# Optimization experiments

Measured on AMD Instinct MI355X. Metric: run time of the kernel, lower is better.

The kernel has to match this reference:

```python
import jax, jax.numpy as jnp
import numpy as np

B, M, E, H = 256, 196, 1024, 8
Dh = E // H          # 128 = att_mid_dim[0]
MID = 64             # att_mid_dim[1]
ALPHA = 1.3          # CELU alpha
EPS = 1e-5


def group_norm(x, w, b, groups=H, eps=EPS):
    # x: [N, C]; torch GroupNorm over channel groups
    N, C = x.shape
    xg = x.reshape(N, groups, C // groups)
    mu = xg.mean(-1, keepdims=True)
    var = xg.var(-1, keepdims=True)
    xn = ((xg - mu) * jax.lax.rsqrt(var + eps)).reshape(N, C)
    return xn * w + b


def proj(x, W, b, gw, gb):
    # Linear -> CELU(1.3) -> GroupNorm(H)
    return group_norm(jax.nn.celu(x @ W + b, alpha=ALPHA), gw, gb)


def setup_inputs() -> dict:
    key0 = jax.random.key(0)
    ks = jax.random.split(key0, 16)
    d = {}
    d["query"] = jax.random.normal(ks[0], (B, E), jnp.float32)
    d["key"] = jax.random.normal(ks[1], (B, M, E), jnp.float32)
    d["mask"] = jax.random.randint(ks[2], (B, M), 0, 2, jnp.int32)
    d["value1"] = jax.random.normal(ks[3], (B, E), jnp.float32)
    d["value2"] = jax.random.normal(ks[4], (B, M, E), jnp.float32)
    s = 0.02
    for i, nm in enumerate(["q", "k", "v1", "v2"]):
        d[f"W{nm}"] = jax.random.normal(ks[5 + i], (E, E), jnp.float32) * s
        d[f"b{nm}"] = jnp.zeros((E,), jnp.float32)
        d[f"g{nm}_w"] = jnp.ones((E,), jnp.float32)
        d[f"g{nm}_b"] = jnp.zeros((E,), jnp.float32)
    d["Wb"] = jax.random.normal(ks[9], (Dh, MID), jnp.float32) * s
    d["bb"] = jnp.zeros((MID,), jnp.float32)
    d["Ws"] = jax.random.normal(ks[10], (MID, 1), jnp.float32) * s
    d["bs"] = jnp.zeros((1,), jnp.float32)
    d["Wc"] = jax.random.normal(ks[11], (MID, Dh), jnp.float32) * s
    d["bc"] = jnp.zeros((Dh,), jnp.float32)
    return d


def reference(query, key, mask, value1, value2,
              Wq, bq, gq_w, gq_b, Wk, bk, gk_w, gk_b,
              Wv1, bv1, gv1_w, gv1_b, Wv2, bv2, gv2_w, gv2_b,
              Wb, bb, Ws, bs, Wc, bc):
    # input projections (dropout layers are identity at eval)
    q = proj(query, Wq, bq, gq_w, gq_b).reshape(B, H, Dh)
    v1 = proj(value1, Wv1, bv1, gv1_w, gv1_b).reshape(B, H, Dh)
    k = proj(key.reshape(-1, E), Wk, bk, gk_w, gk_b).reshape(B, M, H, Dh).transpose(0, 2, 1, 3)   # [B,H,M,Dh]
    v2 = proj(value2.reshape(-1, E), Wv2, bv2, gv2_w, gv2_b).reshape(B, M, H, Dh).transpose(0, 2, 1, 3)

    # SCAttDec
    att_map = q[:, :, None, :] * k                                # [B,H,M,Dh]
    hidden = jax.nn.relu(att_map @ Wb + bb)                       # [B,H,M,MID]
    maskf = mask.astype(hidden.dtype)                             # [B,M]
    mext = maskf[:, None, :, None]                                # [B,1,M,1]
    att_map_pool = jnp.sum(hidden * mext, axis=2) / jnp.sum(mext, axis=2)   # [B,H,MID]

    alpha_spatial = (hidden @ Ws + bs)[..., 0]                    # [B,H,M]
    alpha_spatial = jnp.where(mask[:, None, :] == 0, -1e9, alpha_spatial)
    alpha_spatial = jax.nn.softmax(alpha_spatial, axis=-1)
    v2_pooled = jnp.einsum("bhm,bhmd->bhd", alpha_spatial, v2)    # [B,H,Dh]

    alpha_channel = jax.nn.sigmoid(att_map_pool @ Wc + bc)        # [B,H,Dh]
    attn = v1 * v2_pooled * alpha_channel                         # [B,H,Dh]
    return attn.reshape(B, H * Dh)
```

## Files before the change

### kernel.cpp

```cpp
#include <hip/hip_runtime.h>

typedef unsigned short u16;
typedef unsigned int u32;
typedef __attribute__((ext_vector_type(8))) short short8;
typedef __attribute__((ext_vector_type(4))) float floatx4;

#define E_ 1024
#define B_ 256
#define M_ 196
#define H_ 8
#define DH_ 128
#define MID_ 64

__device__ __forceinline__ u16 f2bf(float f){
  union { float f; u32 u; } v; v.f = f;
  return (u16)((v.u + (((v.u >> 16) & 1u) + 0x7fffu)) >> 16);
}
__device__ __forceinline__ float bf2f(u16 h){
  union { u32 u; float f; } v; v.u = ((u32)h) << 16;
  return v.f;
}
__device__ __forceinline__ u32 pack_bf2(float a, float b){
  u32 ua = __float_as_uint(a) + 0x8000u;
  u32 ub = __float_as_uint(b) + 0x8000u;
  return __builtin_amdgcn_perm(ub, ua, 0x07060302);
}
__device__ __forceinline__ void gl_lds16(const void* g, void* l){
  __builtin_amdgcn_global_load_lds(
      (const __attribute__((address_space(1))) u32*)g,
      (__attribute__((address_space(3))) u32*)l, 16, 0, 0);
}

__global__ __launch_bounds__(256) void wconv_kernel(
    const float* __restrict__ Wq, const float* __restrict__ Wk,
    const float* __restrict__ Wv1, const float* __restrict__ Wv2,
    u16* __restrict__ Wt)
{
  __shared__ u16 tile[64][72];
  const float* W = (blockIdx.z == 0) ? Wq : (blockIdx.z == 1) ? Wk
                 : (blockIdx.z == 2) ? Wv1 : Wv2;
  u16* out = Wt + (size_t)blockIdx.z * (E_ * E_);
  int k0 = blockIdx.x * 64, c0 = blockIdx.y * 64;
  int tx = threadIdx.x & 63, ty = threadIdx.x >> 6;
  #pragma unroll
  for (int i = 0; i < 16; i++){
    int k = ty * 16 + i;
    tile[k][tx] = f2bf(W[(size_t)(k0 + k) * E_ + c0 + tx]);
  }
  __syncthreads();
  #pragma unroll
  for (int i = 0; i < 16; i++){
    int c = ty * 16 + i;
    out[(size_t)(c0 + c) * E_ + k0 + tx] = tile[tx][c];
  }
}

__global__ __launch_bounds__(256, 2) void proj_kernel(
    const float* __restrict__ query, const float* __restrict__ key,
    const float* __restrict__ value1, const float* __restrict__ value2,
    const float* __restrict__ bq, const float* __restrict__ gqw, const float* __restrict__ gqb,
    const float* __restrict__ bk, const float* __restrict__ gkw, const float* __restrict__ gkb,
    const float* __restrict__ bv1, const float* __restrict__ gv1w, const float* __restrict__ gv1b,
    const float* __restrict__ bv2, const float* __restrict__ gv2w, const float* __restrict__ gv2b,
    const u16* __restrict__ Wt,
    u16* __restrict__ qout, u16* __restrict__ kout,
    u16* __restrict__ v1out, u16* __restrict__ v2out)
{
  __shared__ float a_lds[128 * 32];
  __shared__ u16  b_lds[256 * 32];

  const int tid = threadIdx.x;
  const int w = tid >> 6, lane = tid & 63, qd = lane >> 4, lr = lane & 15;
  const int rh = w >> 1, ch = w & 1;

  const int mtb = blockIdx.y;
  const float* X; const float *bias, *gw, *gb; u16* out; int row0, matsel;
  if (mtb < 392)      { X = key;    bias = bk;  gw = gkw;  gb = gkb;  out = kout;  row0 = mtb * 128;         matsel = 1; }
  else if (mtb < 784) { X = value2; bias = bv2; gw = gv2w; gb = gv2b; out = v2out; row0 = (mtb - 392) * 128; matsel = 3; }
  else if (mtb < 786) { X = query;  bias = bq;  gw = gqw;  gb = gqb;  out = qout;  row0 = (mtb - 784) * 128; matsel = 0; }
  else                { X = value1; bias = bv1; gw = gv1w; gb = gv1b; out = v1out; row0 = (mtb - 786) * 128; matsel = 2; }
  const int col0 = blockIdx.x * 256;

  const int arow_l = w * 32 + (lane >> 3);
  const int aswz   = ((lane & 7) ^ (lane >> 3)) * 4;
  const float* aSrc = X + (size_t)(row0 + arow_l) * E_ + aswz;
  const int bcol_l = w * 64 + (lane >> 2);
  const u16* bSrc = Wt + (size_t)matsel * (E_ * E_) + (size_t)(col0 + bcol_l) * E_ + (lane & 3) * 8;

  floatx4 acc[4][8];
  #pragma unroll
  for (int i = 0; i < 4; i++)
    #pragma unroll
    for (int j = 0; j < 8; j++){
      floatx4 z = {0.f, 0.f, 0.f, 0.f};
      acc[i][j] = z;
    }

  for (int kt = 0; kt < 32; kt++){
    const int k0 = kt * 32;
    __syncthreads();
    #pragma unroll
    for (int c = 0; c < 4; c++)
      gl_lds16(aSrc + (size_t)c * 8 * E_ + k0, &a_lds[(w * 32 + c * 8) * 32]);
    #pragma unroll
    for (int c = 0; c < 4; c++)
      gl_lds16(bSrc + (size_t)c * 16 * E_ + k0, &b_lds[(w * 64 + c * 16) * 32]);
    __syncthreads();

    short8 bfr[8];
    #pragma unroll
    for (int nt = 0; nt < 8; nt++)
      bfr[nt] = *(const short8*)&b_lds[(ch * 128 + nt * 16 + lr) * 32 + qd * 8];

    const int sw = lr & 7;
    #pragma unroll
    for (int m2 = 0; m2 < 4; m2++){
      const int row = rh * 64 + m2 * 16 + lr;
      float4 f0 = *(const float4*)&a_lds[row * 32 + (((qd << 1)    ) ^ sw) * 4];
      float4 f1 = *(const float4*)&a_lds[row * 32 + (((qd << 1) | 1) ^ sw) * 4];
      union { u32 u[4]; short8 s; } af;
      af.u[0] = pack_bf2(f0.x, f0.y);
      af.u[1] = pack_bf2(f0.z, f0.w);
      af.u[2] = pack_bf2(f1.x, f1.y);
      af.u[3] = pack_bf2(f1.z, f1.w);
      #pragma unroll
      for (int nt = 0; nt < 8; nt++)
        acc[m2][nt] = __builtin_amdgcn_mfma_f32_16x16x32_bf16(af.s, bfr[nt], acc[m2][nt], 0, 0, 0);
    }
  }

  float biasv[8], gwv[8], gbv[8];
  #pragma unroll
  for (int nt = 0; nt < 8; nt++){
    int c = col0 + ch * 128 + nt * 16 + lr;
    biasv[nt] = bias[c]; gwv[nt] = gw[c]; gbv[nt] = gb[c];
  }
  #pragma unroll
  for (int m2 = 0; m2 < 4; m2++){
    #pragma unroll
    for (int r = 0; r < 4; r++){
      float s = 0.f, s2 = 0.f;
      #pragma unroll
      for (int nt = 0; nt < 8; nt++){
        float x = acc[m2][nt][r] + biasv[nt];
        x = (x > 0.f) ? x : 1.3f * expm1f(x * (1.0f / 1.3f));
        acc[m2][nt][r] = x;
        s += x; s2 += x * x;
      }
      #pragma unroll
      for (int off = 1; off < 16; off <<= 1){
        s  += __shfl_xor(s,  off, 64);
        s2 += __shfl_xor(s2, off, 64);
      }
      float mean = s * 0.0078125f;
      float var  = s2 * 0.0078125f - mean * mean;
      float rstd = rsqrtf(var + 1e-5f);
      size_t base = (size_t)(row0 + rh * 64 + m2 * 16 + qd * 4 + r) * E_ + col0 + ch * 128;
      #pragma unroll
      for (int nt = 0; nt < 8; nt++)
        out[base + nt * 16 + lr] = f2bf((acc[m2][nt][r] - mean) * rstd * gwv[nt] + gbv[nt]);
    }
  }
}

__global__ __launch_bounds__(256) void attn_kernel(
    const u16* __restrict__ qproj, const u16* __restrict__ kproj,
    const u16* __restrict__ v1proj, const u16* __restrict__ v2proj,
    const int* __restrict__ mask,
    const float* __restrict__ Wb, const float* __restrict__ bb,
    const float* __restrict__ Ws, const float* __restrict__ bs,
    const float* __restrict__ Wc, const float* __restrict__ bc,
    float* __restrict__ outp)
{
  __shared__ u16 wbt[64 * 136];
  __shared__ float qv[128];
  __shared__ float mrow[208];
  __shared__ float logitv[208];
  __shared__ float hsum_l[4][64];
  __shared__ float wexpv[208];
  __shared__ float poolv[64];
  __shared__ float v2acc[4][128];
  __shared__ float red[8];

  const int tid = threadIdx.x;
  const int w = tid >> 6, lane = tid & 63, qd = lane >> 4, lr = lane & 15;
  const int b = blockIdx.y, h = blockIdx.x;

  const u16* kbase  = kproj  + (size_t)b * M_ * E_ + h * DH_;
  const u16* v2base = v2proj + (size_t)b * M_ * E_ + h * DH_;

  if (tid < 128) qv[tid] = bf2f(qproj[(size_t)b * E_ + h * DH_ + tid]);
  if (tid < 208) mrow[tid] = (tid < M_) ? (float)mask[b * M_ + tid] : 0.f;
  __syncthreads();

  {
    int n = tid & 63, kb = (tid >> 6) * 32;
    #pragma unroll
    for (int kk = 0; kk < 32; kk++)
      wbt[n * 136 + kb + kk] = f2bf(qv[kb + kk] * Wb[(kb + kk) * MID_ + n]);
  }
  __syncthreads();

  float wsv[4], bbv[4];
  #pragma unroll
  for (int nt = 0; nt < 4; nt++){ wsv[nt] = Ws[nt * 16 + lr]; bbv[nt] = bb[nt * 16 + lr]; }
  const float bsv = bs[0];
  float hs[4] = {0, 0, 0, 0};

  for (int mt = w; mt < 13; mt += 4){
    int mrow_g = mt * 16 + lr;
    int mcl = (mrow_g < M_) ? mrow_g : (M_ - 1);
    const u16* arow = kbase + (size_t)mcl * E_;
    floatx4 hacc[4];
    #pragma unroll
    for (int nt = 0; nt < 4; nt++){ floatx4 z = {0.f, 0.f, 0.f, 0.f}; hacc[nt] = z; }
    #pragma unroll
    for (int kc = 0; kc < 4; kc++){
      short8 afr = *(const short8*)(arow + kc * 32 + qd * 8);
      #pragma unroll
      for (int nt = 0; nt < 4; nt++){
        short8 bfr = *(const short8*)&wbt[(nt * 16 + lr) * 136 + kc * 32 + qd * 8];
        hacc[nt] = __builtin_amdgcn_mfma_f32_16x16x32_bf16(afr, bfr, hacc[nt], 0, 0, 0);
      }
    }
    float lp[4] = {0, 0, 0, 0};
    #pragma unroll
    for (int nt = 0; nt < 4; nt++){
      #pragma unroll
      for (int r = 0; r < 4; r++){
        float hv = hacc[nt][r] + bbv[nt];
        hv = fmaxf(hv, 0.f);
        lp[r] += hv * wsv[nt];
        hs[nt] += mrow[mt * 16 + qd * 4 + r] * hv;
      }
    }
    #pragma unroll
    for (int r = 0; r < 4; r++){
      float a = lp[r];
      #pragma unroll
      for (int off = 1; off < 16; off <<= 1) a += __shfl_xor(a, off, 64);
      if (lr == 0) logitv[mt * 16 + qd * 4 + r] = a + bsv;
    }
  }
  #pragma unroll
  for (int nt = 0; nt < 4; nt++){
    hs[nt] += __shfl_xor(hs[nt], 16, 64);
    hs[nt] += __shfl_xor(hs[nt], 32, 64);
  }
  if (lane < 16){
    #pragma unroll
    for (int nt = 0; nt < 4; nt++) hsum_l[w][nt * 16 + lane] = hs[nt];
  }
  __syncthreads();

  if (w == 0){
    float s = 0.f;
    for (int m = lane; m < M_; m += 64) s += mrow[m];
    #pragma unroll
    for (int off = 1; off < 64; off <<= 1) s += __shfl_xor(s, off, 64);
    if (lane == 0) red[0] = s;
  } else if (w == 1){
    float mx = -1e30f;
    for (int m = lane; m < M_; m += 64) if (mrow[m] > 0.5f) mx = fmaxf(mx, logitv[m]);
    #pragma unroll
    for (int off = 1; off < 64; off <<= 1) mx = fmaxf(mx, __shfl_xor(mx, off, 64));
    if (lane == 0) red[1] = mx;
  } else if (w == 2){
    poolv[lane & 63] = hsum_l[0][lane & 63] + hsum_l[1][lane & 63]
                     + hsum_l[2][lane & 63] + hsum_l[3][lane & 63];
  }
  __syncthreads();
  const float cnt = red[0], mx = red[1];
  if (tid < 208)
    wexpv[tid] = (tid < M_ && mrow[tid] > 0.5f) ? expf(logitv[tid] - mx) : 0.f;
  __syncthreads();
  if (w == 0){
    float s = 0.f;
    for (int m = lane; m < M_; m += 64) s += wexpv[m];
    #pragma unroll
    for (int off = 1; off < 64; off <<= 1) s += __shfl_xor(s, off, 64);
    if (lane == 0) red[2] = s;
  } else if (w == 1){
    poolv[lane & 63] = poolv[lane & 63] / cnt;
  }
  __syncthreads();
  const float S = red[2];

  {
    float ac[8] = {0, 0, 0, 0, 0, 0, 0, 0};
    #pragma unroll
    for (int it = 0; it < 13; it++){
      int m = it * 16 + w * 4 + qd;
      if (m < M_){
        float we = wexpv[m];
        uint4 u = *(const uint4*)(v2base + (size_t)m * E_ + lr * 8);
        ac[0] += we * bf2f((u16)(u.x & 0xffff));
        ac[1] += we * bf2f((u16)(u.x >> 16));
        ac[2] += we * bf2f((u16)(u.y & 0xffff));
        ac[3] += we * bf2f((u16)(u.y >> 16));
        ac[4] += we * bf2f((u16)(u.z & 0xffff));
        ac[5] += we * bf2f((u16)(u.z >> 16));
        ac[6] += we * bf2f((u16)(u.w & 0xffff));
        ac[7] += we * bf2f((u16)(u.w >> 16));
      }
    }
    #pragma unroll
    for (int j = 0; j < 8; j++){
      ac[j] += __shfl_xor(ac[j], 16, 64);
      ac[j] += __shfl_xor(ac[j], 32, 64);
    }
    if (qd == 0){
      #pragma unroll
      for (int j = 0; j < 8; j++) v2acc[w][lr * 8 + j] = ac[j];
    }
  }
  __syncthreads();

  if (tid < 128){
    float a = 0.f;
    #pragma unroll 8
    for (int j = 0; j < 64; j++) a += poolv[j] * Wc[j * DH_ + tid];
    float acv = 1.f / (1.f + expf(-(a + bc[tid])));
    float vp = (v2acc[0][tid] + v2acc[1][tid] + v2acc[2][tid] + v2acc[3][tid]) / S;
    float o = bf2f(v1proj[(size_t)b * E_ + h * DH_ + tid]) * vp * acv;
    outp[(size_t)b * E_ + h * DH_ + tid] = o;
  }
}

extern "C" void kernel_launch(void* const* d_in, const int* in_sizes, int n_in,
                              void* d_out, int out_size, void* d_ws, size_t ws_size,
                              hipStream_t stream)
{
  const float* query  = (const float*)d_in[0];
  const float* key    = (const float*)d_in[1];
  const int*   mask   = (const int*)d_in[2];
  const float* value1 = (const float*)d_in[3];
  const float* value2 = (const float*)d_in[4];
  const float* Wq  = (const float*)d_in[5];
  const float* bq  = (const float*)d_in[6];
  const float* gqw = (const float*)d_in[7];
  const float* gqb = (const float*)d_in[8];
  const float* Wk  = (const float*)d_in[9];
  const float* bk  = (const float*)d_in[10];
  const float* gkw = (const float*)d_in[11];
  const float* gkb = (const float*)d_in[12];
  const float* Wv1 = (const float*)d_in[13];
  const float* bv1 = (const float*)d_in[14];
  const float* gv1w= (const float*)d_in[15];
  const float* gv1b= (const float*)d_in[16];
  const float* Wv2 = (const float*)d_in[17];
  const float* bv2 = (const float*)d_in[18];
  const float* gv2w= (const float*)d_in[19];
  const float* gv2b= (const float*)d_in[20];
  const float* Wb  = (const float*)d_in[21];
  const float* bb  = (const float*)d_in[22];
  const float* Ws  = (const float*)d_in[23];
  const float* bs  = (const float*)d_in[24];
  const float* Wc  = (const float*)d_in[25];
  const float* bc  = (const float*)d_in[26];

  const size_t NK = (size_t)B_ * M_;
  u16* kout  = (u16*)d_ws;
  u16* v2out = kout  + NK * E_;
  u16* qout  = v2out + NK * E_;
  u16* v1out = qout  + (size_t)B_ * E_;
  u16* Wt    = v1out + (size_t)B_ * E_;

  dim3 g0(16, 16, 4);
  wconv_kernel<<<g0, 256, 0, stream>>>(Wq, Wk, Wv1, Wv2, Wt);

  dim3 g1(4, 788);
  proj_kernel<<<g1, 256, 0, stream>>>(query, key, value1, value2,
      bq, gqw, gqb, bk, gkw, gkb, bv1, gv1w, gv1b, bv2, gv2w, gv2b,
      Wt, qout, kout, v1out, v2out);

  dim3 g2(H_, B_);
  attn_kernel<<<g2, 256, 0, stream>>>(qout, kout, v1out, v2out, mask,
      Wb, bb, Ws, bs, Wc, bc, (float*)d_out);
}
```

Before: 886.2 us.

## Retile projection GEMM to 128x128 with register-staged bf16 A tiles

The projection GEMM tile shrinks from 128x256 to 128x128 output and the K step grows from 32 to 64. The fp32 A operand is now prefetched into registers, converted to bf16 once per tile, and stored to LDS with an XOR swizzle. Previously each wave reconverted fp32 from LDS on every use. Because each 128-column group now spans two waves, GroupNorm statistics are combined through shared memory, and occupancy is raised to 3 blocks per CU. The cost is twice as many blocks, so the A matrix is read from global memory twice as often, plus an extra barrier in the epilogue.

```diff
diff --git a/kernel.cpp b/kernel.cpp
--- a/kernel.cpp
+++ b/kernel.cpp
@@ -55,7 +55,7 @@
   }
 }
 
-__global__ __launch_bounds__(256, 2) void proj_kernel(
+__global__ __launch_bounds__(256, 3) void proj_kernel(
     const float* __restrict__ query, const float* __restrict__ key,
     const float* __restrict__ value1, const float* __restrict__ value2,
     const float* __restrict__ bq, const float* __restrict__ gqw, const float* __restrict__ gqb,
@@ -66,8 +66,9 @@
     u16* __restrict__ qout, u16* __restrict__ kout,
     u16* __restrict__ v1out, u16* __restrict__ v2out)
 {
-  __shared__ float a_lds[128 * 32];
-  __shared__ u16  b_lds[256 * 32];
+  __shared__ u16 a_lds[128 * 64];
+  __shared__ u16 b_lds[128 * 64];
+  __shared__ float ps[128][2][2];
 
   const int tid = threadIdx.x;
   const int w = tid >> 6, lane = tid & 63, qd = lane >> 4, lr = lane & 15;
@@ -79,60 +80,69 @@
   else if (mtb < 784) { X = value2; bias = bv2; gw = gv2w; gb = gv2b; out = v2out; row0 = (mtb - 392) * 128; matsel = 3; }
   else if (mtb < 786) { X = query;  bias = bq;  gw = gqw;  gb = gqb;  out = qout;  row0 = (mtb - 784) * 128; matsel = 0; }
   else                { X = value1; bias = bv1; gw = gv1w; gb = gv1b; out = v1out; row0 = (mtb - 786) * 128; matsel = 2; }
-  const int col0 = blockIdx.x * 256;
-
-  const int arow_l = w * 32 + (lane >> 3);
-  const int aswz   = ((lane & 7) ^ (lane >> 3)) * 4;
-  const float* aSrc = X + (size_t)(row0 + arow_l) * E_ + aswz;
-  const int bcol_l = w * 64 + (lane >> 2);
-  const u16* bSrc = Wt + (size_t)matsel * (E_ * E_) + (size_t)(col0 + bcol_l) * E_ + (lane & 3) * 8;
-
-  floatx4 acc[4][8];
+  const int col0 = blockIdx.x * 128;
+
+  const int ar = tid >> 1, ah = tid & 1, rsw = ar & 7;
+  const float* aSrc = X + (size_t)(row0 + ar) * E_ + ah * 32;
+  const u16* bSrc = Wt + (size_t)matsel * (E_ * E_)
+                  + (size_t)(col0 + w * 32 + (lane >> 3)) * E_
+                  + ((lane & 7) ^ (lane >> 3)) * 8;
+
+  floatx4 acc[4][4];
   #pragma unroll
   for (int i = 0; i < 4; i++)
     #pragma unroll
-    for (int j = 0; j < 8; j++){
+    for (int j = 0; j < 4; j++){
       floatx4 z = {0.f, 0.f, 0.f, 0.f};
       acc[i][j] = z;
     }
 
-  for (int kt = 0; kt < 32; kt++){
-    const int k0 = kt * 32;
+  float4 aRegs[8];
+  #pragma unroll
+  for (int j = 0; j < 8; j++) aRegs[j] = *(const float4*)(aSrc + j * 4);
+
+  for (int kt = 0; kt < 16; kt++){
+    const int k0 = kt * 64;
     __syncthreads();
     #pragma unroll
     for (int c = 0; c < 4; c++)
-      gl_lds16(aSrc + (size_t)c * 8 * E_ + k0, &a_lds[(w * 32 + c * 8) * 32]);
-    #pragma unroll
-    for (int c = 0; c < 4; c++)
-      gl_lds16(bSrc + (size_t)c * 16 * E_ + k0, &b_lds[(w * 64 + c * 16) * 32]);
+      gl_lds16(bSrc + (size_t)c * 8 * E_ + k0, &b_lds[(w * 32 + c * 8) * 64]);
+    #pragma unroll
+    for (int j2 = 0; j2 < 4; j2++){
+      union { u32 u[4]; int4 v; } pk;
+      pk.u[0] = pack_bf2(aRegs[j2 * 2].x,     aRegs[j2 * 2].y);
+      pk.u[1] = pack_bf2(aRegs[j2 * 2].z,     aRegs[j2 * 2].w);
+      pk.u[2] = pack_bf2(aRegs[j2 * 2 + 1].x, aRegs[j2 * 2 + 1].y);
+      pk.u[3] = pack_bf2(aRegs[j2 * 2 + 1].z, aRegs[j2 * 2 + 1].w);
+      *(int4*)&a_lds[ar * 64 + (((ah * 4 + j2) ^ rsw)) * 8] = pk.v;
+    }
     __syncthreads();
-
-    short8 bfr[8];
-    #pragma unroll
-    for (int nt = 0; nt < 8; nt++)
-      bfr[nt] = *(const short8*)&b_lds[(ch * 128 + nt * 16 + lr) * 32 + qd * 8];
-
-    const int sw = lr & 7;
-    #pragma unroll
-    for (int m2 = 0; m2 < 4; m2++){
-      const int row = rh * 64 + m2 * 16 + lr;
-      float4 f0 = *(const float4*)&a_lds[row * 32 + (((qd << 1)    ) ^ sw) * 4];
-      float4 f1 = *(const float4*)&a_lds[row * 32 + (((qd << 1) | 1) ^ sw) * 4];
-      union { u32 u[4]; short8 s; } af;
-      af.u[0] = pack_bf2(f0.x, f0.y);
-      af.u[1] = pack_bf2(f0.z, f0.w);
-      af.u[2] = pack_bf2(f1.x, f1.y);
-      af.u[3] = pack_bf2(f1.z, f1.w);
-      #pragma unroll
-      for (int nt = 0; nt < 8; nt++)
-        acc[m2][nt] = __builtin_amdgcn_mfma_f32_16x16x32_bf16(af.s, bfr[nt], acc[m2][nt], 0, 0, 0);
-    }
-  }
-
-  float biasv[8], gwv[8], gbv[8];
-  #pragma unroll
-  for (int nt = 0; nt < 8; nt++){
-    int c = col0 + ch * 128 + nt * 16 + lr;
+    if (kt < 15){
+      #pragma unroll
+      for (int j = 0; j < 8; j++)
+        aRegs[j] = *(const float4*)(aSrc + k0 + 64 + j * 4);
+    }
+    #pragma unroll
+    for (int kk = 0; kk < 2; kk++){
+      const int cs = kk * 4 + qd;
+      short8 bfr[4];
+      #pragma unroll
+      for (int nt = 0; nt < 4; nt++)
+        bfr[nt] = *(const short8*)&b_lds[(ch * 64 + nt * 16 + lr) * 64 + (cs ^ (lr & 7)) * 8];
+      #pragma unroll
+      for (int m2 = 0; m2 < 4; m2++){
+        short8 afr = *(const short8*)&a_lds[(rh * 64 + m2 * 16 + lr) * 64 + (cs ^ (lr & 7)) * 8];
+        #pragma unroll
+        for (int nt = 0; nt < 4; nt++)
+          acc[m2][nt] = __builtin_amdgcn_mfma_f32_16x16x32_bf16(afr, bfr[nt], acc[m2][nt], 0, 0, 0);
+      }
+    }
+  }
+
+  float biasv[4], gwv[4], gbv[4];
+  #pragma unroll
+  for (int nt = 0; nt < 4; nt++){
+    int c = col0 + ch * 64 + nt * 16 + lr;
     biasv[nt] = bias[c]; gwv[nt] = gw[c]; gbv[nt] = gb[c];
   }
   #pragma unroll
@@ -141,7 +151,7 @@
     for (int r = 0; r < 4; r++){
       float s = 0.f, s2 = 0.f;
       #pragma unroll
-      for (int nt = 0; nt < 8; nt++){
+      for (int nt = 0; nt < 4; nt++){
         float x = acc[m2][nt][r] + biasv[nt];
         x = (x > 0.f) ? x : 1.3f * expm1f(x * (1.0f / 1.3f));
         acc[m2][nt][r] = x;
@@ -152,12 +162,26 @@
         s  += __shfl_xor(s,  off, 64);
         s2 += __shfl_xor(s2, off, 64);
       }
+      if (lr == 0){
+        int row = rh * 64 + m2 * 16 + qd * 4 + r;
+        ps[row][ch][0] = s; ps[row][ch][1] = s2;
+      }
+    }
+  }
+  __syncthreads();
+  #pragma unroll
+  for (int m2 = 0; m2 < 4; m2++){
+    #pragma unroll
+    for (int r = 0; r < 4; r++){
+      int row = rh * 64 + m2 * 16 + qd * 4 + r;
+      float s  = ps[row][0][0] + ps[row][1][0];
+      float s2 = ps[row][0][1] + ps[row][1][1];
       float mean = s * 0.0078125f;
       float var  = s2 * 0.0078125f - mean * mean;
       float rstd = rsqrtf(var + 1e-5f);
-      size_t base = (size_t)(row0 + rh * 64 + m2 * 16 + qd * 4 + r) * E_ + col0 + ch * 128;
-      #pragma unroll
-      for (int nt = 0; nt < 8; nt++)
+      size_t base = (size_t)(row0 + row) * E_ + col0 + ch * 64;
+      #pragma unroll
+      for (int nt = 0; nt < 4; nt++)
         out[base + nt * 16 + lr] = f2bf((acc[m2][nt][r] - mean) * rstd * gwv[nt] + gbv[nt]);
     }
   }
@@ -369,7 +393,7 @@
   dim3 g0(16, 16, 4);
   wconv_kernel<<<g0, 256, 0, stream>>>(Wq, Wk, Wv1, Wv2, Wt);
 
-  dim3 g1(4, 788);
+  dim3 g1(8, 788);
   proj_kernel<<<g1, 256, 0, stream>>>(query, key, value1, value2,
       bq, gqw, gqb, bk, gkw, gkb, bv1, gv1w, gv1b, bv2, gv2w, gv2b,
       Wt, qout, kout, v1out, v2out);
```

Result: slower. 1.037 ms (+17.1%).
